# Kernel tuning notes

Hardware: AMD Instinct MI355X
Metric: run time of the kernel (lower is better)

Reference implementation:

```python
import jax, jax.numpy as jnp
import numpy as np

# Mamba-2 dims (from wrapper: d_model=hidden_size=2048, d_state=64, d_conv=4, expand=2, headdim=64)
D_MODEL = 2048
EXPAND = 2
HEADDIM = 64
D_STATE = 64
D_CONV = 4
D_INNER = EXPAND * D_MODEL            # 4096
NHEADS = D_INNER // HEADDIM           # 64
NGROUPS = 1                           # mamba_ssm default
CONV_DIM = D_INNER + 2 * NGROUPS * D_STATE          # 4224
D_IN_PROJ = 2 * D_INNER + 2 * NGROUPS * D_STATE + NHEADS  # 8384
BATCH = 1
SEQLEN = 1024
RMS_EPS = 1e-5


def setup_inputs() -> dict:
    key = jax.random.key(0)
    ks = jax.random.split(key, 8)
    x = jax.random.normal(ks[0], (BATCH, SEQLEN, D_MODEL), jnp.float32)
    W_in = jax.random.normal(ks[1], (D_IN_PROJ, D_MODEL), jnp.float32) * 0.02
    conv_w = jax.random.normal(ks[2], (CONV_DIM, D_CONV), jnp.float32) * 0.2
    conv_b = jnp.zeros((CONV_DIM,), jnp.float32)
    # dt_bias so that softplus(dt_raw + dt_bias) lands in a realistic dt range ~[1e-3, 5e-2]
    dt_bias = jax.random.uniform(ks[3], (NHEADS,), jnp.float32, -6.0, -3.0)
    # A = -exp(A_log), A_log init like mamba_ssm: A ~ Uniform(1, 16)
    A_log = jnp.log(1.0 + 15.0 * jax.random.uniform(ks[4], (NHEADS,), jnp.float32))
    D = jnp.ones((NHEADS,), jnp.float32)
    norm_w = jnp.ones((D_INNER,), jnp.float32)
    W_out = jax.random.normal(ks[5], (D_MODEL, D_INNER), jnp.float32) * 0.02
    return {"x": x, "W_in": W_in, "conv_w": conv_w, "conv_b": conv_b,
            "dt_bias": dt_bias, "A_log": A_log, "D": D, "norm_w": norm_w, "W_out": W_out}


def reference(x, W_in, conv_w, conv_b, dt_bias, A_log, D, norm_w, W_out):
    B, T, _ = x.shape
    # input projection -> [z | xBC | dt]
    zxbcdt = jnp.einsum('btd,pd->btp', x, W_in)
    z = zxbcdt[..., :D_INNER]                                  # [B,T,D_INNER] gate
    xBC = zxbcdt[..., D_INNER:D_INNER + CONV_DIM]              # [B,T,CONV_DIM]
    dt = jax.nn.softplus(zxbcdt[..., D_INNER + CONV_DIM:] + dt_bias)  # [B,T,H]
    # causal depthwise conv1d (kernel D_CONV) + SiLU
    xp = jnp.pad(xBC, ((0, 0), (D_CONV - 1, 0), (0, 0)))
    conv = conv_b + sum(xp[:, k:k + T, :] * conv_w[:, k] for k in range(D_CONV))
    xBC = jax.nn.silu(conv)
    xh = xBC[..., :D_INNER].reshape(B, T, NHEADS, HEADDIM)     # [B,T,H,P]
    Bm = xBC[..., D_INNER:D_INNER + D_STATE]                   # [B,T,N] (ngroups=1)
    Cm = xBC[..., D_INNER + D_STATE:]                          # [B,T,N]
    A = -jnp.exp(A_log)                                        # [H], negative
    dA = jnp.exp(dt * A)                                       # [B,T,H] decay per step

    def step(h, inp):
        # h: [B,H,P,N]
        dA_t, dt_t, B_t, x_t, C_t = inp
        h = h * dA_t[:, :, None, None] + jnp.einsum('bh,bn,bhp->bhpn', dt_t, B_t, x_t)
        y_t = jnp.einsum('bhpn,bn->bhp', h, C_t)
        return h, y_t

    h0 = jnp.zeros((B, NHEADS, HEADDIM, D_STATE), x.dtype)
    xs = (dA.transpose(1, 0, 2), dt.transpose(1, 0, 2), Bm.transpose(1, 0, 2),
          xh.transpose(1, 0, 2, 3), Cm.transpose(1, 0, 2))
    _, ys = jax.lax.scan(step, h0, xs)                         # ys: [T,B,H,P]
    y = ys.transpose(1, 0, 2, 3) + D[None, None, :, None] * xh  # skip term D*x
    y = y.reshape(B, T, D_INNER)
    # gated RMSNorm (norm_before_gate=False): norm(y * silu(z)) * weight
    y = y * jax.nn.silu(z)
    y = y * jax.lax.rsqrt(jnp.mean(y * y, axis=-1, keepdims=True) + RMS_EPS) * norm_w
    return jnp.einsum('bti,di->btd', y, W_out)
```

## Files before the change

kernel.cpp:

```cpp
#include <hip/hip_runtime.h>
#include <hip/hip_bf16.h>
#include <stdint.h>

#define SEQLEN   1024
#define DMODEL   2048
#define DINNER   4096
#define NHEADS   64
#define HEADDIM  64
#define DSTATE   64
#define CONVDIM  4224
#define DINPROJ  8384
#define RMS_EPS  1e-5f
#define CPAD     68
#define LP       72

typedef __attribute__((ext_vector_type(8))) __bf16 bf16x8;
typedef __attribute__((ext_vector_type(8))) unsigned short us8;
typedef __attribute__((ext_vector_type(4))) float f32x4;

__device__ __forceinline__ ushort f2bf(float f) {
    uint32_t u = __float_as_uint(f);
    u += 0x7FFFu + ((u >> 16) & 1u);
    return (ushort)(u >> 16);
}

__device__ __forceinline__ float bf2f(ushort u) {
    return __uint_as_float((uint32_t)u << 16);
}

__device__ __forceinline__ float silu(float a) { return a / (1.f + __expf(-a)); }

__device__ __forceinline__ void gload_lds16(const void* g, void* l) {
    __builtin_amdgcn_global_load_lds(
        (const __attribute__((address_space(1))) void*)g,
        (__attribute__((address_space(3))) void*)l, 16, 0, 0);
}

__global__ __launch_bounds__(256) void cvt1_kernel(const float* __restrict__ in,
                                                   ushort* __restrict__ out, int n4) {
    int i = blockIdx.x * 256 + threadIdx.x;
    if (i < n4) {
        float4 v = ((const float4*)in)[i];
        ushort4 o;
        o.x = f2bf(v.x); o.y = f2bf(v.y); o.z = f2bf(v.z); o.w = f2bf(v.w);
        ((ushort4*)out)[i] = o;
    }
}

__global__ __launch_bounds__(256, 3) void gemm4_bf16_nt(
    const __bf16* __restrict__ A, const float* __restrict__ B,
    float* __restrict__ C, int M, int N, int K,
    int ntx, int nty, int nk, int ksteps, int swz)
{
    __shared__ __align__(16) __bf16 As[2][128 * 32];
    __shared__ __align__(16) float  Bsf[2][128 * 32];
    const int tid  = threadIdx.x;
    const int lane = tid & 63;
    const int wave = tid >> 6;
    const int wr = wave >> 1, wc = wave & 1;
    int id = blockIdx.x;
    if (swz) { int q = (ntx * nty * nk) >> 3; id = (id & 7) * q + (id >> 3); }
    const int kz  = id / (ntx * nty);
    const int rem = id % (ntx * nty);
    const int tx = rem / nty, ty = rem % nty;
    const int row0 = ty * 128, col0 = tx * 128;
    const int lr = lane & 15, lq = lane >> 4;
    const int rA = lane >> 2, jl = lane & 3;
    const int k0 = kz * ksteps * 32;

    const __bf16* srcA[2];
    int dstA[2];
    #pragma unroll
    for (int e = 0; e < 2; ++e) {
        int r0 = (wave * 2 + e) * 16;
        int r  = r0 + rA;
        int jg = jl ^ ((rA >> 1) & 3);
        srcA[e] = A + (size_t)(row0 + r) * K + k0 + jg * 8;
        dstA[e] = r0 * 32;
    }
    const float* srcB[4];
    int dstBb[4];
    #pragma unroll
    for (int p = 0; p < 4; ++p) {
        int rbase = p * 32 + wave * 8;
        int r  = rbase + (lane >> 3);
        int jg = (lane & 7) ^ (lane >> 3);
        int gb = col0 + r; if (gb > N - 1) gb = N - 1;
        srcB[p]  = B + (size_t)gb * K + k0 + jg * 4;
        dstBb[p] = rbase * 32;
    }

    f32x4 acc[4][4] = {};
    const int nt = ksteps;

#define STAGE(BUF)                                                            \
    _Pragma("unroll")                                                         \
    for (int e = 0; e < 2; ++e) {                                             \
        gload_lds16(srcA[e], &As[BUF][dstA[e]]);                              \
        srcA[e] += 32;                                                        \
    }                                                                         \
    _Pragma("unroll")                                                         \
    for (int p = 0; p < 4; ++p) {                                             \
        gload_lds16(srcB[p], &Bsf[BUF][dstBb[p]]);                            \
        srcB[p] += 32;                                                        \
    }

#define COMPUTE(BUF)                                                          \
    {                                                                         \
        bf16x8 af[4], bfr[4];                                                 \
        const int slA = (lq ^ ((lr >> 1) & 3)) * 8;                           \
        _Pragma("unroll")                                                     \
        for (int m = 0; m < 4; ++m) {                                         \
            int r = wr * 64 + m * 16 + lr;                                    \
            af[m] = *(const bf16x8*)(&As[BUF][r * 32 + slA]);                 \
        }                                                                     \
        _Pragma("unroll")                                                     \
        for (int n = 0; n < 4; ++n) {                                         \
            int r = wc * 64 + n * 16 + lr;                                    \
            float4 f0 = *(const float4*)(&Bsf[BUF][r * 32 + (((2*lq)   ^ (r & 7)) * 4)]); \
            float4 f1 = *(const float4*)(&Bsf[BUF][r * 32 + (((2*lq+1) ^ (r & 7)) * 4)]); \
            bf16x8 v;                                                         \
            v[0] = (__bf16)f0.x; v[1] = (__bf16)f0.y;                         \
            v[2] = (__bf16)f0.z; v[3] = (__bf16)f0.w;                         \
            v[4] = (__bf16)f1.x; v[5] = (__bf16)f1.y;                         \
            v[6] = (__bf16)f1.z; v[7] = (__bf16)f1.w;                         \
            bfr[n] = v;                                                       \
        }                                                                     \
        __builtin_amdgcn_s_setprio(1);                                        \
        _Pragma("unroll")                                                     \
        for (int m = 0; m < 4; ++m)                                           \
            _Pragma("unroll")                                                 \
            for (int n = 0; n < 4; ++n)                                       \
                acc[m][n] = __builtin_amdgcn_mfma_f32_16x16x32_bf16(af[m], bfr[n], acc[m][n], 0, 0, 0); \
        __builtin_amdgcn_s_setprio(0);                                        \
    }

    STAGE(0);
    asm volatile("s_waitcnt vmcnt(0)" ::: "memory");
    __builtin_amdgcn_s_barrier();
    asm volatile("" ::: "memory");

    for (int t = 0; t < nt; t += 2) {
        STAGE(1);
        COMPUTE(0);
        asm volatile("s_waitcnt vmcnt(0)" ::: "memory");
        __builtin_amdgcn_s_barrier();
        asm volatile("" ::: "memory");
        if (t + 2 < nt) { STAGE(0); }
        COMPUTE(1);
        asm volatile("s_waitcnt vmcnt(0)" ::: "memory");
        __builtin_amdgcn_s_barrier();
        asm volatile("" ::: "memory");
    }
#undef STAGE
#undef COMPUTE

    float* Co = C + (size_t)kz * M * N;
    #pragma unroll
    for (int m = 0; m < 4; ++m)
        #pragma unroll
        for (int n = 0; n < 4; ++n) {
            int col = col0 + wc * 64 + n * 16 + lr;
            if (col < N) {
                #pragma unroll
                for (int j = 0; j < 4; ++j) {
                    int row = row0 + wr * 64 + m * 16 + lq * 4 + j;
                    Co[(size_t)row * N + col] = acc[m][n][j];
                }
            }
        }
}

__global__ __launch_bounds__(256) void reduce4_scale_kernel(
    const float* __restrict__ p, const float* __restrict__ ssbuf,
    float* __restrict__ out, int n4)
{
    int i = blockIdx.x * 256 + threadIdx.x;
    if (i < n4) {
        int t = i >> 9;
        float sc = rsqrtf(ssbuf[t] * (1.f / DINNER) + RMS_EPS);
        float4 a = ((const float4*)p)[i];
        float4 b = ((const float4*)p)[i + n4];
        float4 c = ((const float4*)p)[i + 2 * (size_t)n4];
        float4 d = ((const float4*)p)[i + 3 * (size_t)n4];
        float4 o = {(a.x + b.x + c.x + d.x) * sc, (a.y + b.y + c.y + d.y) * sc,
                    (a.z + b.z + c.z + d.z) * sc, (a.w + b.w + c.w + d.w) * sc};
        ((float4*)out)[i] = o;
    }
}

__global__ __launch_bounds__(256, 3) void chunk_intra_kernel(
    const float* __restrict__ zx, const float* __restrict__ conv_w,
    const float* __restrict__ conv_b, const float* __restrict__ dt_bias,
    const float* __restrict__ A_log,
    float* __restrict__ x_scan, float* __restrict__ Cb,
    float* __restrict__ yintra, float* __restrict__ Tc, float* __restrict__ Ssum)
{
    const int head  = blockIdx.x >> 4;
    const int chunk = blockIdx.x & 15;
    const int t0 = chunk * 64;
    const int tid = threadIdx.x;
    const int lane = tid & 63, wv = tid >> 6;
    const int lr = lane & 15, lq = lane >> 4;

    __shared__ __align__(16) ushort XT [64 * LP];
    __shared__ __align__(16) ushort Crm[64 * LP];
    __shared__ __align__(16) ushort Brm[64 * LP];
    __shared__ __align__(16) ushort BnT[64 * LP];
    __shared__ __align__(16) ushort Grm[64 * LP];
    __shared__ float Sc[64], dts[64], ws[64];

    {
        const int p = lane;
        const int c = head * 64 + p;
        const float w0 = conv_w[c*4+0], w1 = conv_w[c*4+1];
        const float w2 = conv_w[c*4+2], w3 = conv_w[c*4+3];
        const float bia = conv_b[c];
        const int gt0 = t0 + wv * 16;
        const float* zc = zx + DINNER + c;
        float xm3 = (gt0 >= 3) ? zc[(size_t)(gt0-3)*DINPROJ] : 0.f;
        float xm2 = (gt0 >= 2) ? zc[(size_t)(gt0-2)*DINPROJ] : 0.f;
        float xm1 = (gt0 >= 1) ? zc[(size_t)(gt0-1)*DINPROJ] : 0.f;
        uint32_t pk[8];
        #pragma unroll
        for (int e = 0; e < 16; ++e) {
            float xt = zc[(size_t)(gt0+e)*DINPROJ];
            float s  = silu(bia + xm3*w0 + xm2*w1 + xm1*w2 + xt*w3);
            x_scan[(size_t)(gt0+e)*DINNER + c] = s;
            ushort b = f2bf(s);
            if (e & 1) pk[e>>1] |= (uint32_t)b << 16; else pk[e>>1] = (uint32_t)b;
            xm3 = xm2; xm2 = xm1; xm1 = xt;
        }
        int4 lo = { (int)pk[0], (int)pk[1], (int)pk[2], (int)pk[3] };
        int4 hi = { (int)pk[4], (int)pk[5], (int)pk[6], (int)pk[7] };
        *(int4*)&XT[p * LP + wv*16]     = lo;
        *(int4*)&XT[p * LP + wv*16 + 8] = hi;
    }

    #pragma unroll
    for (int k = 0; k < 4; ++k) {
        int n0 = wv * 16 + k * 4;
        int gt = t0 + lane;
        {
            float4 w0 = *(const float4*)&conv_w[(4096 + n0 + 0) * 4];
            float4 w1 = *(const float4*)&conv_w[(4096 + n0 + 1) * 4];
            float4 w2 = *(const float4*)&conv_w[(4096 + n0 + 2) * 4];
            float4 w3 = *(const float4*)&conv_w[(4096 + n0 + 3) * 4];
            float4 bv = *(const float4*)&conv_b[4096 + n0];
            float4 r0 = {0,0,0,0}, r1 = {0,0,0,0}, r2 = {0,0,0,0}, r3;
            const float* base = zx + (size_t)gt * DINPROJ + 8192 + n0;
            if (gt >= 3) r0 = *(const float4*)(base - 3 * DINPROJ);
            if (gt >= 2) r1 = *(const float4*)(base - 2 * DINPROJ);
            if (gt >= 1) r2 = *(const float4*)(base - 1 * DINPROJ);
            r3 = *(const float4*)base;
            ushort b0 = f2bf(silu(bv.x + r0.x*w0.x + r1.x*w0.y + r2.x*w0.z + r3.x*w0.w));
            ushort b1 = f2bf(silu(bv.y + r0.y*w1.x + r1.y*w1.y + r2.y*w1.z + r3.y*w1.w));
            ushort b2 = f2bf(silu(bv.z + r0.z*w2.x + r1.z*w2.y + r2.z*w2.z + r3.z*w2.w));
            ushort b3 = f2bf(silu(bv.w + r0.w*w3.x + r1.w*w3.y + r2.w*w3.z + r3.w*w3.w));
            uint2 pk = { (uint32_t)b0 | ((uint32_t)b1 << 16),
                         (uint32_t)b2 | ((uint32_t)b3 << 16) };
            *(uint2*)&Brm[lane * LP + n0] = pk;
            BnT[(n0+0)*LP + lane] = b0; BnT[(n0+1)*LP + lane] = b1;
            BnT[(n0+2)*LP + lane] = b2; BnT[(n0+3)*LP + lane] = b3;
        }
        {
            float4 w0 = *(const float4*)&conv_w[(4160 + n0 + 0) * 4];
            float4 w1 = *(const float4*)&conv_w[(4160 + n0 + 1) * 4];
            float4 w2 = *(const float4*)&conv_w[(4160 + n0 + 2) * 4];
            float4 w3 = *(const float4*)&conv_w[(4160 + n0 + 3) * 4];
            float4 bv = *(const float4*)&conv_b[4160 + n0];
            float4 r0 = {0,0,0,0}, r1 = {0,0,0,0}, r2 = {0,0,0,0}, r3;
            const float* base = zx + (size_t)gt * DINPROJ + 8256 + n0;
            if (gt >= 3) r0 = *(const float4*)(base - 3 * DINPROJ);
            if (gt >= 2) r1 = *(const float4*)(base - 2 * DINPROJ);
            if (gt >= 1) r2 = *(const float4*)(base - 1 * DINPROJ);
            r3 = *(const float4*)base;
            float4 cv;
            cv.x = silu(bv.x + r0.x*w0.x + r1.x*w0.y + r2.x*w0.z + r3.x*w0.w);
            cv.y = silu(bv.y + r0.y*w1.x + r1.y*w1.y + r2.y*w1.z + r3.y*w1.w);
            cv.z = silu(bv.z + r0.z*w2.x + r1.z*w2.y + r2.z*w2.z + r3.z*w2.w);
            cv.w = silu(bv.w + r0.w*w3.x + r1.w*w3.y + r2.w*w3.z + r3.w*w3.w);
            uint2 pk = { (uint32_t)f2bf(cv.x) | ((uint32_t)f2bf(cv.y) << 16),
                         (uint32_t)f2bf(cv.z) | ((uint32_t)f2bf(cv.w) << 16) };
            *(uint2*)&Crm[lane * LP + n0] = pk;
            if (head == 0) *(float4*)&Cb[(size_t)gt * 64 + n0] = cv;
        }
    }

    if (wv == 1) {
        float raw = zx[(size_t)(t0 + lane) * DINPROJ + 8320 + head] + dt_bias[head];
        float dt  = (raw > 20.f) ? raw : log1pf(__expf(raw));
        dts[lane] = dt;
        float v = dt * (-__expf(A_log[head]));
        #pragma unroll
        for (int off = 1; off < 64; off <<= 1) {
            float u = __shfl_up(v, off, 64);
            if (lane >= off) v += u;
        }
        Sc[lane] = v;
        Ssum[(t0 + lane) * 64 + head] = v;
    }
    __syncthreads();
    if (tid < 64) ws[tid] = dts[tid] * __expf(Sc[63] - Sc[tid]);

    const int i0 = wv * 16;
    f32x4 gf[4] = {};
    #pragma unroll
    for (int kk = 0; kk < 2; ++kk) {
        bf16x8 a = __builtin_bit_cast(bf16x8,
            *(const us8*)&Crm[(i0 + lr) * LP + lq*8 + kk*32]);
        #pragma unroll
        for (int f = 0; f < 4; ++f) {
            bf16x8 b = __builtin_bit_cast(bf16x8,
                *(const us8*)&Brm[(f*16 + lr) * LP + lq*8 + kk*32]);
            gf[f] = __builtin_amdgcn_mfma_f32_16x16x32_bf16(a, b, gf[f], 0, 0, 0);
        }
    }
    {
        float Si[4];
        #pragma unroll
        for (int j = 0; j < 4; ++j) Si[j] = Sc[i0 + lq*4 + j];
        #pragma unroll
        for (int f = 0; f < 4; ++f) {
            int s = f*16 + lr;
            float dw = dts[s], Ss_ = Sc[s];
            #pragma unroll
            for (int j = 0; j < 4; ++j) {
                int i = i0 + lq*4 + j;
                float v = (s <= i) ? gf[f][j] * dw * __expf(Si[j] - Ss_) : 0.f;
                Grm[i * LP + s] = f2bf(v);
            }
        }
    }
    __syncthreads();

    const int p0 = i0;
    bf16x8 xa[2], xw[2];
    #pragma unroll
    for (int kk = 0; kk < 2; ++kk) {
        us8 raw = *(const us8*)&XT[(p0 + lr) * LP + lq*8 + kk*32];
        xa[kk] = __builtin_bit_cast(bf16x8, raw);
        us8 sw;
        #pragma unroll
        for (int e = 0; e < 8; ++e) {
            int s = lq*8 + kk*32 + e;
            sw[e] = f2bf(bf2f(raw[e]) * ws[s]);
        }
        xw[kk] = __builtin_bit_cast(bf16x8, sw);
    }
    f32x4 yf[4] = {};
    f32x4 tf[4] = {};
    #pragma unroll
    for (int kk = 0; kk < 2; ++kk) {
        #pragma unroll
        for (int f = 0; f < 4; ++f) {
            bf16x8 gb = __builtin_bit_cast(bf16x8,
                *(const us8*)&Grm[(f*16 + lr) * LP + lq*8 + kk*32]);
            yf[f] = __builtin_amdgcn_mfma_f32_16x16x32_bf16(xa[kk], gb, yf[f], 0, 0, 0);
            bf16x8 bb = __builtin_bit_cast(bf16x8,
                *(const us8*)&BnT[(f*16 + lr) * LP + lq*8 + kk*32]);
            tf[f] = __builtin_amdgcn_mfma_f32_16x16x32_bf16(xw[kk], bb, tf[f], 0, 0, 0);
        }
    }
    float* tcb = Tc + (size_t)(head * 16 + chunk) * 4096;
    #pragma unroll
    for (int f = 0; f < 4; ++f) {
        int col = f*16 + lr;
        int p   = p0 + lq*4;
        float4 yv = {yf[f][0], yf[f][1], yf[f][2], yf[f][3]};
        *(float4*)&yintra[(size_t)(t0 + col) * DINNER + head*64 + p] = yv;
        #pragma unroll
        for (int j = 0; j < 4; ++j)
            tcb[(p + j) * 64 + col] = tf[f][j];
    }
}

__global__ __launch_bounds__(256) void chunk_state_kernel(
    float* __restrict__ Tc, const float* __restrict__ Ssum)
{
    const int head = blockIdx.x;
    const int tid = threadIdx.x;
    float h[16] = {};
    float* base = Tc + (size_t)head * 16 * 4096 + tid * 16;
    for (int c = 0; c < 16; ++c) {
        float Q = __expf(Ssum[(c * 64 + 63) * 64 + head]);
        float4* p = (float4*)(base + (size_t)c * 4096);
        #pragma unroll
        for (int v = 0; v < 4; ++v) {
            float4 t = p[v];
            float4 hold = {h[v*4], h[v*4+1], h[v*4+2], h[v*4+3]};
            h[v*4+0] = h[v*4+0] * Q + t.x;
            h[v*4+1] = h[v*4+1] * Q + t.y;
            h[v*4+2] = h[v*4+2] * Q + t.z;
            h[v*4+3] = h[v*4+3] * Q + t.w;
            p[v] = hold;
        }
    }
}

__global__ __launch_bounds__(256) void inter_combine_kernel(
    const float* __restrict__ Hpre, const float* __restrict__ Cb,
    const float* __restrict__ Ssum, const float* __restrict__ yintra,
    const float* __restrict__ x_scan, const float* __restrict__ zx,
    const float* __restrict__ Dv, const float* __restrict__ norm_w,
    ushort* __restrict__ ybf, float* __restrict__ ssbuf)
{
    const int head  = blockIdx.x >> 4;
    const int chunk = blockIdx.x & 15;
    const int t0 = chunk * 64;
    const int tid = threadIdx.x;
    const int ty = tid >> 4, tx = tid & 15;
    const int lane = tid & 63, wv = tid >> 6;

    __shared__ __align__(16) float HsT[64][CPAD];
    __shared__ __align__(16) float CsT[64][CPAD];
    __shared__ float Se[64];

    const float* hb = Hpre + (size_t)(head * 16 + chunk) * 4096;
    #pragma unroll
    for (int k = 0; k < 4; ++k) {
        int n0 = wv * 16 + k * 4;
        float4 h = *(const float4*)&hb[lane * 64 + n0];
        float4 c = *(const float4*)&Cb[(t0 + lane) * 64 + n0];
        HsT[n0][lane] = h.x; HsT[n0+1][lane] = h.y; HsT[n0+2][lane] = h.z; HsT[n0+3][lane] = h.w;
        CsT[n0][lane] = c.x; CsT[n0+1][lane] = c.y; CsT[n0+2][lane] = c.z; CsT[n0+3][lane] = c.w;
    }
    if (tid < 64) Se[tid] = __expf(Ssum[(t0 + tid) * 64 + head]);
    __syncthreads();

    float acc[4][4] = {};
    for (int n = 0; n < 64; ++n) {
        float4 ci = *(const float4*)&CsT[n][ty * 4];
        float4 hp = *(const float4*)&HsT[n][tx * 4];
        acc[0][0] += ci.x*hp.x; acc[0][1] += ci.x*hp.y; acc[0][2] += ci.x*hp.z; acc[0][3] += ci.x*hp.w;
        acc[1][0] += ci.y*hp.x; acc[1][1] += ci.y*hp.y; acc[1][2] += ci.y*hp.z; acc[1][3] += ci.y*hp.w;
        acc[2][0] += ci.z*hp.x; acc[2][1] += ci.z*hp.y; acc[2][2] += ci.z*hp.z; acc[2][3] += ci.z*hp.w;
        acc[3][0] += ci.w*hp.x; acc[3][1] += ci.w*hp.y; acc[3][2] += ci.w*hp.z; acc[3][3] += ci.w*hp.w;
    }

    const float Dh = Dv[head];
    const int col = head * 64 + tx * 4;
    float4 nw = *(const float4*)&norm_w[col];
    float ssp[4];
    #pragma unroll
    for (int di = 0; di < 4; ++di) {
        int t = t0 + ty * 4 + di;
        float se = Se[ty * 4 + di];
        float4 yi = *(const float4*)&yintra[(size_t)t * DINNER + col];
        float4 xh = *(const float4*)&x_scan[(size_t)t * DINNER + col];
        float4 zv = *(const float4*)&zx[(size_t)t * DINPROJ + col];
        float4 y;
        y.x = (acc[di][0] * se + yi.x + Dh * xh.x) * silu(zv.x);
        y.y = (acc[di][1] * se + yi.y + Dh * xh.y) * silu(zv.y);
        y.z = (acc[di][2] * se + yi.z + Dh * xh.z) * silu(zv.z);
        y.w = (acc[di][3] * se + yi.w + Dh * xh.w) * silu(zv.w);
        ssp[di] = y.x*y.x + y.y*y.y + y.z*y.z + y.w*y.w;
        ushort4 o;
        o.x = f2bf(y.x * nw.x); o.y = f2bf(y.y * nw.y);
        o.z = f2bf(y.z * nw.z); o.w = f2bf(y.w * nw.w);
        *(ushort4*)&ybf[(size_t)t * DINNER + col] = o;
    }
    #pragma unroll
    for (int di = 0; di < 4; ++di) {
        float s = ssp[di];
        s += __shfl_xor(s, 1, 64);
        s += __shfl_xor(s, 2, 64);
        s += __shfl_xor(s, 4, 64);
        s += __shfl_xor(s, 8, 64);
        if (tx == 0) atomicAdd(&ssbuf[t0 + ty * 4 + di], s);
    }
}

extern "C" void kernel_launch(void* const* d_in, const int* in_sizes, int n_in,
                              void* d_out, int out_size, void* d_ws, size_t ws_size,
                              hipStream_t stream)
{
    const float* x       = (const float*)d_in[0];
    const float* W_in    = (const float*)d_in[1];
    const float* conv_w  = (const float*)d_in[2];
    const float* conv_b  = (const float*)d_in[3];
    const float* dt_bias = (const float*)d_in[4];
    const float* A_log   = (const float*)d_in[5];
    const float* Dv      = (const float*)d_in[6];
    const float* norm_w  = (const float*)d_in[7];
    const float* W_out   = (const float*)d_in[8];
    float* out = (float*)d_out;

    char* ws = (char*)d_ws;
    const size_t OFF_WIN  = 0;
    const size_t OFF_WOUT = 34340864;
    const size_t OFF_XBF  = OFF_WOUT + 16777216;
    const size_t OFF_ZX   = OFF_XBF + 4194304;
    const size_t OFF_XSC  = OFF_ZX + 34340864;
    const size_t OFF_CB   = OFF_XSC + 16777216;
    const size_t OFF_SSB  = OFF_CB + 262144;
    const size_t OFF_YBF  = OFF_SSB + 4096;
    const size_t OFF_TC   = OFF_YBF + 8388608;
    const size_t OFF_SS   = OFF_TC + 16777216;

    ushort* xBf    = (ushort*)(ws + OFF_XBF);
    float*  zxb    = (float*)(ws + OFF_ZX);
    float*  xsc    = (float*)(ws + OFF_XSC);
    float*  Cb     = (float*)(ws + OFF_CB);
    float*  ssbuf  = (float*)(ws + OFF_SSB);
    ushort* ybf    = (ushort*)(ws + OFF_YBF);
    float*  Tc     = (float*)(ws + OFF_TC);
    float*  Ssum   = (float*)(ws + OFF_SS);
    float*  yintra = (float*)(ws + OFF_WIN);
    float*  part   = (float*)(ws + OFF_WIN);

    const int nX4 = SEQLEN * DMODEL / 4;
    cvt1_kernel<<<(nX4 + 255) / 256, 256, 0, stream>>>(x, xBf, nX4);

    hipMemsetAsync(ssbuf, 0, SEQLEN * sizeof(float), stream);

    gemm4_bf16_nt<<<528, 256, 0, stream>>>(
        (const __bf16*)xBf, W_in, zxb,
        SEQLEN, DINPROJ, DMODEL, 66, 8, 1, DMODEL / 32, 1);

    chunk_intra_kernel<<<1024, 256, 0, stream>>>(
        zxb, conv_w, conv_b, dt_bias, A_log, xsc, Cb, yintra, Tc, Ssum);

    chunk_state_kernel<<<64, 256, 0, stream>>>(Tc, Ssum);

    inter_combine_kernel<<<1024, 256, 0, stream>>>(
        Tc, Cb, Ssum, yintra, xsc, zxb, Dv, norm_w, ybf, ssbuf);

    gemm4_bf16_nt<<<512, 256, 0, stream>>>(
        (const __bf16*)ybf, W_out, part,
        SEQLEN, DMODEL, DINNER, 16, 8, 4, DINNER / 32 / 4, 1);

    reduce4_scale_kernel<<<(SEQLEN * DMODEL / 4 + 255) / 256, 256, 0, stream>>>(
        part, ssbuf, out, SEQLEN * DMODEL / 4);
}
```

Measured before the change: 180.3 us.

## Convert GEMM B tile to bf16 once in LDS before MFMA reads

The fp32 B tile is now converted to bf16 once per k-step by all threads into a separate swizzled LDS buffer. Previously each wave converted the fp32 values itself during every compute, so the same conversion was repeated across waves and fp32 operands were read from LDS. B staging drops to a single fp32 buffer, which cuts LDS use and lets launch bounds request 4 blocks per CU instead of 3. In exchange, each k-step gains an extra barrier and LDS write pass, and with single-buffered B the global load for the next step can no longer overlap the conversion in the same way.

```diff
diff --git a/kernel.cpp b/kernel.cpp
--- a/kernel.cpp
+++ b/kernel.cpp
@@ -47,13 +47,14 @@
     }
 }
 
-__global__ __launch_bounds__(256, 3) void gemm4_bf16_nt(
+__global__ __launch_bounds__(256, 4) void gemm4_bf16_nt(
     const __bf16* __restrict__ A, const float* __restrict__ B,
     float* __restrict__ C, int M, int N, int K,
     int ntx, int nty, int nk, int ksteps, int swz)
 {
     __shared__ __align__(16) __bf16 As[2][128 * 32];
-    __shared__ __align__(16) float  Bsf[2][128 * 32];
+    __shared__ __align__(16) ushort Bsu[128 * 32];
+    __shared__ __align__(16) float  Bsf[128 * 32];
     const int tid  = threadIdx.x;
     const int lane = tid & 63;
     const int wave = tid >> 6;
@@ -79,52 +80,57 @@
         dstA[e] = r0 * 32;
     }
     const float* srcB[4];
-    int dstBb[4];
+    int dstBf[4];
+    const int rB  = lane >> 3;
+    const int jg4 = (lane & 7) ^ rB;
     #pragma unroll
     for (int p = 0; p < 4; ++p) {
         int rbase = p * 32 + wave * 8;
-        int r  = rbase + (lane >> 3);
-        int jg = (lane & 7) ^ (lane >> 3);
-        int gb = col0 + r; if (gb > N - 1) gb = N - 1;
-        srcB[p]  = B + (size_t)gb * K + k0 + jg * 4;
-        dstBb[p] = rbase * 32;
+        int gb = col0 + rbase + rB; if (gb > N - 1) gb = N - 1;
+        srcB[p]  = B + (size_t)gb * K + k0 + jg4 * 4;
+        dstBf[p] = rbase * 32;
     }
 
     f32x4 acc[4][4] = {};
     const int nt = ksteps;
 
-#define STAGE(BUF)                                                            \
+#define STAGE(ABUF)                                                           \
     _Pragma("unroll")                                                         \
     for (int e = 0; e < 2; ++e) {                                             \
-        gload_lds16(srcA[e], &As[BUF][dstA[e]]);                              \
+        gload_lds16(srcA[e], &As[ABUF][dstA[e]]);                             \
         srcA[e] += 32;                                                        \
     }                                                                         \
     _Pragma("unroll")                                                         \
     for (int p = 0; p < 4; ++p) {                                             \
-        gload_lds16(srcB[p], &Bsf[BUF][dstBb[p]]);                            \
+        gload_lds16(srcB[p], &Bsf[dstBf[p]]);                                 \
         srcB[p] += 32;                                                        \
     }
 
-#define COMPUTE(BUF)                                                          \
+#define CVT()                                                                 \
+    _Pragma("unroll")                                                         \
+    for (int p = 0; p < 4; ++p) {                                             \
+        float4 f = *(const float4*)&Bsf[(p * 32 + wave * 8) * 32 + lane * 4]; \
+        int r = p * 32 + wave * 8 + rB;                                       \
+        int slot8 = (jg4 >> 1) ^ ((r >> 1) & 3);                              \
+        uint2 pk = { (uint32_t)f2bf(f.x) | ((uint32_t)f2bf(f.y) << 16),       \
+                     (uint32_t)f2bf(f.z) | ((uint32_t)f2bf(f.w) << 16) };     \
+        *(uint2*)&Bsu[r * 32 + slot8 * 8 + (jg4 & 1) * 4] = pk;               \
+    }
+
+#define COMPUTE(ABUF)                                                         \
     {                                                                         \
         bf16x8 af[4], bfr[4];                                                 \
         const int slA = (lq ^ ((lr >> 1) & 3)) * 8;                           \
         _Pragma("unroll")                                                     \
         for (int m = 0; m < 4; ++m) {                                         \
             int r = wr * 64 + m * 16 + lr;                                    \
-            af[m] = *(const bf16x8*)(&As[BUF][r * 32 + slA]);                 \
+            af[m] = *(const bf16x8*)(&As[ABUF][r * 32 + slA]);                \
         }                                                                     \
         _Pragma("unroll")                                                     \
         for (int n = 0; n < 4; ++n) {                                         \
             int r = wc * 64 + n * 16 + lr;                                    \
-            float4 f0 = *(const float4*)(&Bsf[BUF][r * 32 + (((2*lq)   ^ (r & 7)) * 4)]); \
-            float4 f1 = *(const float4*)(&Bsf[BUF][r * 32 + (((2*lq+1) ^ (r & 7)) * 4)]); \
-            bf16x8 v;                                                         \
-            v[0] = (__bf16)f0.x; v[1] = (__bf16)f0.y;                         \
-            v[2] = (__bf16)f0.z; v[3] = (__bf16)f0.w;                         \
-            v[4] = (__bf16)f1.x; v[5] = (__bf16)f1.y;                         \
-            v[6] = (__bf16)f1.z; v[7] = (__bf16)f1.w;                         \
-            bfr[n] = v;                                                       \
+            int sl = (lq ^ ((r >> 1) & 3)) * 8;                               \
+            bfr[n] = __builtin_bit_cast(bf16x8, *(const us8*)(&Bsu[r * 32 + sl])); \
         }                                                                     \
         __builtin_amdgcn_s_setprio(1);                                        \
         _Pragma("unroll")                                                     \
@@ -140,19 +146,19 @@
     __builtin_amdgcn_s_barrier();
     asm volatile("" ::: "memory");
 
-    for (int t = 0; t < nt; t += 2) {
-        STAGE(1);
-        COMPUTE(0);
+    for (int t = 0; t < nt; ++t) {
+        CVT();
+        asm volatile("s_waitcnt lgkmcnt(0)" ::: "memory");
+        __builtin_amdgcn_s_barrier();
+        asm volatile("" ::: "memory");
+        if (t + 1 < nt) { STAGE((t + 1) & 1); }
+        COMPUTE(t & 1);
         asm volatile("s_waitcnt vmcnt(0)" ::: "memory");
         __builtin_amdgcn_s_barrier();
         asm volatile("" ::: "memory");
-        if (t + 2 < nt) { STAGE(0); }
-        COMPUTE(1);
-        asm volatile("s_waitcnt vmcnt(0)" ::: "memory");
-        __builtin_amdgcn_s_barrier();
-        asm volatile("" ::: "memory");
     }
 #undef STAGE
+#undef CVT
 #undef COMPUTE
 
     float* Co = C + (size_t)kz * M * N;
```

After: 212.5 us. 17.9% more time.
